# Kernel tuning notes

Hardware: AMD Instinct MI355X
Metric: run time of the kernel (lower is better)

The kernel has to match this reference:

```python
import jax, jax.numpy as jnp
import numpy as np

N, E, IN_DIM, OUT_DIM, R = 100000, 1600000, 128, 128, 8


def setup_inputs() -> dict:
    key = jax.random.key(0)
    k = jax.random.split(key, 6)
    scale_rel = np.sqrt(6.0 / (IN_DIM + OUT_DIM))  # xavier_uniform bound
    x = jax.random.normal(k[0], (N, IN_DIM), dtype=jnp.float32)
    edge_index = jax.random.randint(k[1], (2, E), 0, N, dtype=jnp.int64)
    edge_type = jax.random.randint(k[2], (E,), 0, R, dtype=jnp.int64)
    rel_weight = jax.random.uniform(k[3], (R, IN_DIM, OUT_DIM), dtype=jnp.float32,
                                    minval=-scale_rel, maxval=scale_rel)
    w_self = jax.random.uniform(k[4], (IN_DIM, OUT_DIM), dtype=jnp.float32,
                                minval=-scale_rel, maxval=scale_rel)
    b_self = jax.random.normal(k[5], (OUT_DIM,), dtype=jnp.float32) * 0.01
    return {"x": x, "edge_index": edge_index, "edge_type": edge_type,
            "rel_weight": rel_weight, "w_self": w_self, "b_self": b_self}


def reference(x, edge_index, edge_type, rel_weight, w_self, b_self):
    n = x.shape[0]
    src, dst = edge_index[0], edge_index[1]
    # self-loop term: W_self @ h_v + b
    out = x @ w_self + b_self                                  # (N, out)
    # pre-transform every node by every relation, then gather per edge.
    # equivalent to per-relation masked (x[src_r] @ W_r) + scatter_add.
    xw = jnp.einsum('ni,rio->nro', x, rel_weight)               # (N, R, out)
    msg = xw[src, edge_type]                                    # (E, out)
    agg = jax.ops.segment_sum(msg, dst, num_segments=n)         # (N, out)
    deg = jax.ops.segment_sum(jnp.ones(dst.shape[0], x.dtype), dst, num_segments=n)
    deg = jnp.clip(deg, 1.0)[:, None]                           # (N, 1)
    return jax.nn.relu(out + agg / deg)
```

## Files before the change

### kernel.cpp

```cpp
#include <hip/hip_runtime.h>
#include <hip/hip_bf16.h>

typedef __attribute__((ext_vector_type(4))) float f32x4_t;
typedef __attribute__((ext_vector_type(8))) short bf16x8_t;

#define NCLS 8

__device__ __forceinline__ float bf2f(ushort u) {
  return __uint_as_float(((unsigned)u) << 16);
}
__device__ __forceinline__ ushort f2bf(float f) {
  unsigned u = __float_as_uint(f);
  u += 0x7fffu + ((u >> 16) & 1u);
  return (ushort)(u >> 16);
}
__device__ __forceinline__ uint packbf2(float x, float y) {
  return (uint)f2bf(x) | ((uint)f2bf(y) << 16);
}

__global__ void deg2_kernel(const int* __restrict__ dst, int* __restrict__ deg2,
                            int N, long E) {
  long i = (long)blockIdx.x * blockDim.x + threadIdx.x;
  long st = (long)gridDim.x * blockDim.x;
  for (; i < E; i += st) {
    int cls = (int)((i >> 8) & (NCLS - 1));
    atomicAdd(&deg2[(size_t)cls * N + dst[i]], 1);
  }
}

__global__ void nodedeg_kernel(const int* __restrict__ deg2, int* __restrict__ nodedeg, int N) {
  int d = blockIdx.x * 256 + threadIdx.x;
  if (d >= N) return;
  int s = 0;
#pragma unroll
  for (int c = 0; c < NCLS; c++) s += deg2[(size_t)c * N + d];
  nodedeg[d] = s;
}

__global__ __launch_bounds__(256) void scan1(const int* __restrict__ deg, int* __restrict__ starts,
                                             int* __restrict__ bsum, int M) {
  __shared__ int lds[256];
  const int tid = threadIdx.x;
  const int base = blockIdx.x * 1024 + tid * 4;
  int v0 = 0, v1 = 0, v2 = 0, v3 = 0;
  if (base + 3 < M) {
    int4 q = *(const int4*)(deg + base);
    v0 = q.x; v1 = q.y; v2 = q.z; v3 = q.w;
  } else {
    if (base + 0 < M) v0 = deg[base];
    if (base + 1 < M) v1 = deg[base + 1];
    if (base + 2 < M) v2 = deg[base + 2];
    if (base + 3 < M) v3 = deg[base + 3];
  }
  int s = v0 + v1 + v2 + v3;
  lds[tid] = s;
  __syncthreads();
  for (int off = 1; off < 256; off <<= 1) {
    int t = (tid >= off) ? lds[tid - off] : 0;
    __syncthreads();
    lds[tid] += t;
    __syncthreads();
  }
  int p = lds[tid] - s;
  if (tid == 255) bsum[blockIdx.x] = lds[255];
  if (base + 0 < M) starts[base + 0] = p; p += v0;
  if (base + 1 < M) starts[base + 1] = p; p += v1;
  if (base + 2 < M) starts[base + 2] = p; p += v2;
  if (base + 3 < M) starts[base + 3] = p;
}

__global__ __launch_bounds__(256) void scan2(int* __restrict__ bsum, int nb) {
  __shared__ int lds[256];
  const int tid = threadIdx.x;
  const int base = tid * 4;
  int v[4];
#pragma unroll
  for (int j = 0; j < 4; j++) v[j] = (base + j < nb) ? bsum[base + j] : 0;
  int s = v[0] + v[1] + v[2] + v[3];
  lds[tid] = s;
  __syncthreads();
  for (int off = 1; off < 256; off <<= 1) {
    int t = (tid >= off) ? lds[tid - off] : 0;
    __syncthreads();
    lds[tid] += t;
    __syncthreads();
  }
  int p = lds[tid] - s;
#pragma unroll
  for (int j = 0; j < 4; j++) {
    if (base + j < nb) bsum[base + j] = p;
    p += v[j];
  }
}

__global__ void scan3(int* __restrict__ starts, const int* __restrict__ bsum, int M) {
  int i = blockIdx.x * 256 + threadIdx.x;
  if (i < M) starts[i] += bsum[i >> 10];
}

__global__ void cursor_init(const int* __restrict__ deg2, const int* __restrict__ node_starts,
                            int* __restrict__ cursor, int N) {
  int d = blockIdx.x * 256 + threadIdx.x;
  if (d >= N) return;
  int run = node_starts[d];
#pragma unroll
  for (int c = 0; c < NCLS; c++) {
    cursor[(size_t)c * N + d] = run;
    run += deg2[(size_t)c * N + d];
  }
}

__global__ void fill_csr(const int* __restrict__ src, const int* __restrict__ dst,
                         const int* __restrict__ et, int* __restrict__ cursor,
                         uint* __restrict__ packed, int N, long E) {
  long i = (long)blockIdx.x * blockDim.x + threadIdx.x;
  long st = (long)gridDim.x * blockDim.x;
  for (; i < E; i += st) {
    int cls = (int)((i >> 8) & (NCLS - 1));
    int pos = atomicAdd(&cursor[(size_t)cls * N + dst[i]], 1);
    packed[pos] = ((uint)src[i] << 4) | (uint)et[i];
  }
}

__global__ void build_wT(const float* __restrict__ rel, const float* __restrict__ wself,
                         ushort* __restrict__ wT, int R) {
  int id = blockIdx.x * blockDim.x + threadIdx.x;
  int total = (R + 1) * 128 * 128;
  if (id >= total) return;
  int r = id >> 14;
  int rem = id & 16383;
  int o = rem >> 7;
  int i = rem & 127;
  float v = (r < R) ? rel[((size_t)r << 14) + (i << 7) + o] : wself[(i << 7) + o];
  wT[id] = f2bf(v);
}

__global__ void conv_x_kernel(const float* __restrict__ x, ushort* __restrict__ xb, long n4) {
  long i = (long)blockIdx.x * blockDim.x + threadIdx.x;
  long st = (long)gridDim.x * blockDim.x;
  for (; i < n4; i += st) {
    float4 v = ((const float4*)x)[i];
    ushort4 o;
    o.x = f2bf(v.x); o.y = f2bf(v.y); o.z = f2bf(v.z); o.w = f2bf(v.w);
    ((ushort4*)xb)[i] = o;
  }
}

__global__ __launch_bounds__(256) void gather_sum(const uint* __restrict__ packed,
                                                  const int* __restrict__ node_starts,
                                                  const int* __restrict__ nodedeg,
                                                  const ushort* __restrict__ xb,
                                                  ushort* __restrict__ S,
                                                  int N) {
  const int lane = threadIdx.x & 63;
  const int d = blockIdx.x * 4 + (threadIdx.x >> 6);
  if (d >= N) return;

  const int s0 = node_starts[d];
  const int dg = nodedeg[d];
  const int e1 = s0 + dg;

  float a0x = 0, a0y = 0, a1x = 0, a1y = 0, a2x = 0, a2y = 0, a3x = 0, a3y = 0;
  float a4x = 0, a4y = 0, a5x = 0, a5y = 0, a6x = 0, a6y = 0, a7x = 0, a7y = 0;

#define ACCUM(t, vx, vy)                                  \
  switch (t) {                                            \
    case 0: a0x += vx; a0y += vy; break;                  \
    case 1: a1x += vx; a1y += vy; break;                  \
    case 2: a2x += vx; a2y += vy; break;                  \
    case 3: a3x += vx; a3y += vy; break;                  \
    case 4: a4x += vx; a4y += vy; break;                  \
    case 5: a5x += vx; a5y += vy; break;                  \
    case 6: a6x += vx; a6y += vy; break;                  \
    default: a7x += vx; a7y += vy; break;                 \
  }

  int e = s0;
  for (; e + 3 < e1; e += 4) {
    uint r0 = packed[e], r1 = packed[e + 1], r2 = packed[e + 2], r3 = packed[e + 3];
    ushort2 m0 = *(const ushort2*)(xb + (size_t)(r0 >> 4) * 128 + lane * 2);
    ushort2 m1 = *(const ushort2*)(xb + (size_t)(r1 >> 4) * 128 + lane * 2);
    ushort2 m2 = *(const ushort2*)(xb + (size_t)(r2 >> 4) * 128 + lane * 2);
    ushort2 m3 = *(const ushort2*)(xb + (size_t)(r3 >> 4) * 128 + lane * 2);
    int t0 = (int)(r0 & 15u), t1 = (int)(r1 & 15u);
    int t2 = (int)(r2 & 15u), t3 = (int)(r3 & 15u);
    ACCUM(t0, bf2f(m0.x), bf2f(m0.y));
    ACCUM(t1, bf2f(m1.x), bf2f(m1.y));
    ACCUM(t2, bf2f(m2.x), bf2f(m2.y));
    ACCUM(t3, bf2f(m3.x), bf2f(m3.y));
  }
  for (; e < e1; e++) {
    uint r0 = packed[e];
    ushort2 m0 = *(const ushort2*)(xb + (size_t)(r0 >> 4) * 128 + lane * 2);
    int t0 = (int)(r0 & 15u);
    ACCUM(t0, bf2f(m0.x), bf2f(m0.y));
  }
#undef ACCUM

  const float inv = 1.0f / (float)((dg > 1) ? dg : 1);
  uint* Sd = (uint*)(S + (size_t)d * 1024) + lane;
  __builtin_nontemporal_store(packbf2(a0x * inv, a0y * inv), Sd + 0 * 64);
  __builtin_nontemporal_store(packbf2(a1x * inv, a1y * inv), Sd + 1 * 64);
  __builtin_nontemporal_store(packbf2(a2x * inv, a2y * inv), Sd + 2 * 64);
  __builtin_nontemporal_store(packbf2(a3x * inv, a3y * inv), Sd + 3 * 64);
  __builtin_nontemporal_store(packbf2(a4x * inv, a4y * inv), Sd + 4 * 64);
  __builtin_nontemporal_store(packbf2(a5x * inv, a5y * inv), Sd + 5 * 64);
  __builtin_nontemporal_store(packbf2(a6x * inv, a6y * inv), Sd + 6 * 64);
  __builtin_nontemporal_store(packbf2(a7x * inv, a7y * inv), Sd + 7 * 64);
}

__global__ __launch_bounds__(512) void agg_gemm(const ushort* __restrict__ S,
                                                const ushort* __restrict__ xb,
                                                const ushort* __restrict__ wT,
                                                const float* __restrict__ b,
                                                float* __restrict__ out,
                                                int N, int NR) {
  __shared__ ushort smem[2][16384];

  const int tid = threadIdx.x;
  const int lane = tid & 63;
  const int wave = tid >> 6;
  const int l15 = lane & 15;
  const int l4 = lane >> 4;
  const int nodebase = blockIdx.x * 256 + wave * 32;

  int nd[2], rd[2];
  nd[0] = nodebase + l15;
  nd[1] = nodebase + 16 + l15;
  rd[0] = (nd[0] < N) ? nd[0] : (N - 1);
  rd[1] = (nd[1] < N) ? nd[1] : (N - 1);

  f32x4_t acc[2][8];
#pragma unroll
  for (int g = 0; g < 2; g++)
#pragma unroll
    for (int nt = 0; nt < 8; nt++) acc[g][nt] = {0.f, 0.f, 0.f, 0.f};

  {
    bf16x8_t sreg[4];
#pragma unroll
    for (int j = 0; j < 4; j++) {
      int c = tid + j * 512;
      sreg[j] = *(const bf16x8_t*)(wT + c * 8);
    }
#pragma unroll
    for (int j = 0; j < 4; j++) {
      int c = tid + j * 512;
      int o = c >> 4;
      int colb = (c & 15) * 16;
      int byte = o * 256 + (colb ^ ((o & 7) << 4));
      *(bf16x8_t*)((char*)smem[0] + byte) = sreg[j];
    }
  }
  __syncthreads();

  for (int r = 0; r < NR; r++) {
    bf16x8_t sf[2][4];
#pragma unroll
    for (int g = 0; g < 2; g++) {
      const ushort* srow = (r < NR - 1) ? (S + ((size_t)rd[g] * 8 + r) * 128 + l4 * 8)
                                        : (xb + (size_t)rd[g] * 128 + l4 * 8);
#pragma unroll
      for (int kk = 0; kk < 4; kk++)
        sf[g][kk] = *(const bf16x8_t*)(srow + kk * 32);
    }

    bf16x8_t sreg[4];
    const bool pf = (r + 1 < NR);
    if (pf) {
      const ushort* wsrc = wT + ((size_t)(r + 1) << 14);
#pragma unroll
      for (int j = 0; j < 4; j++) {
        int c = tid + j * 512;
        sreg[j] = *(const bf16x8_t*)(wsrc + c * 8);
      }
    }

    const char* wbuf = (const char*)smem[r & 1];
#pragma unroll
    for (int nt = 0; nt < 8; nt++) {
      bf16x8_t wf[4];
      const int row = nt * 16 + l15;
      const int swz = (row & 7) << 4;
#pragma unroll
      for (int kk = 0; kk < 4; kk++) {
        int colb = l4 * 16 + kk * 64;
        wf[kk] = *(const bf16x8_t*)(wbuf + row * 256 + (colb ^ swz));
      }
#pragma unroll
      for (int g = 0; g < 2; g++)
#pragma unroll
        for (int kk = 0; kk < 4; kk++)
          acc[g][nt] = __builtin_amdgcn_mfma_f32_16x16x32_bf16(wf[kk], sf[g][kk], acc[g][nt], 0, 0, 0);
    }

    if (pf) {
#pragma unroll
      for (int j = 0; j < 4; j++) {
        int c = tid + j * 512;
        int o = c >> 4;
        int colb = (c & 15) * 16;
        int byte = o * 256 + (colb ^ ((o & 7) << 4));
        *(bf16x8_t*)((char*)smem[(r + 1) & 1] + byte) = sreg[j];
      }
    }
    __syncthreads();
  }

#pragma unroll
  for (int g = 0; g < 2; g++) {
    if (nd[g] < N) {
#pragma unroll
      for (int nt = 0; nt < 8; nt++) {
        float4 bv = *(const float4*)(b + nt * 16 + l4 * 4);
        f32x4_t v = acc[g][nt];
        float4 o;
        o.x = fmaxf(v[0] + bv.x, 0.f);
        o.y = fmaxf(v[1] + bv.y, 0.f);
        o.z = fmaxf(v[2] + bv.z, 0.f);
        o.w = fmaxf(v[3] + bv.w, 0.f);
        *(float4*)(out + (size_t)nd[g] * 128 + nt * 16 + l4 * 4) = o;
      }
    }
  }
}

__global__ void deg_kernel(const int* __restrict__ dst, int* __restrict__ deg, long E) {
  long i = (long)blockIdx.x * blockDim.x + threadIdx.x;
  long st = (long)gridDim.x * blockDim.x;
  for (; i < E; i += st) atomicAdd(&deg[dst[i]], 1);
}
__global__ void naive_edge(const float* __restrict__ x, const int* __restrict__ src,
                           const int* __restrict__ dst, const int* __restrict__ et,
                           const float* __restrict__ rel, float* __restrict__ agg, long E) {
  const int lane = threadIdx.x & 63;
  long wid = ((long)blockIdx.x * blockDim.x + threadIdx.x) >> 6;
  long nw = ((long)gridDim.x * blockDim.x) >> 6;
  for (long e = wid; e < E; e += nw) {
    int s = src[e];
    int d = dst[e];
    int t = et[e];
    const float* xs = x + (size_t)s * 128;
    const float* w = rel + (size_t)t * 128 * 128;
    float a0 = 0.f, a1 = 0.f;
    for (int i = 0; i < 128; i++) {
      float xv = xs[i];
      a0 += xv * w[i * 128 + lane];
      a1 += xv * w[i * 128 + lane + 64];
    }
    atomicAdd(agg + (size_t)d * 128 + lane, a0);
    atomicAdd(agg + (size_t)d * 128 + lane + 64, a1);
  }
}
__global__ void naive_self(const float* __restrict__ x, const float* __restrict__ ws,
                           const float* __restrict__ b, const int* __restrict__ deg,
                           float* __restrict__ out, int N) {
  int v = blockIdx.x;
  int o = threadIdx.x;
  if (v >= N) return;
  const float* xv = x + (size_t)v * 128;
  float acc = b[o];
  for (int i = 0; i < 128; i++) acc += xv[i] * ws[i * 128 + o];
  float dg = (float)max(deg[v], 1);
  float val = acc + out[(size_t)v * 128 + o] / dg;
  out[(size_t)v * 128 + o] = fmaxf(val, 0.f);
}

extern "C" void kernel_launch(void* const* d_in, const int* in_sizes, int n_in,
                              void* d_out, int out_size, void* d_ws, size_t ws_size,
                              hipStream_t stream) {
  const float* x = (const float*)d_in[0];
  const int* ei = (const int*)d_in[1];
  const int* et = (const int*)d_in[2];
  const float* rel = (const float*)d_in[3];
  const float* wself = (const float*)d_in[4];
  const float* bself = (const float*)d_in[5];
  float* out = (float*)d_out;

  const int N = in_sizes[0] / 128;
  const long E = in_sizes[2];
  const int R = in_sizes[3] / (128 * 128);
  const int NR = R + 1;
  const int* srcp = ei;
  const int* dstp = ei + E;

  size_t off = 0;
  auto alloc = [&](size_t bytes) {
    size_t o = off;
    off += (bytes + 255) & ~(size_t)255;
    return o;
  };
  size_t deg2_off = alloc((size_t)NCLS * N * 4);
  size_t nodedeg_off = alloc((size_t)N * 4);
  size_t nstart_off = alloc((size_t)N * 4);
  size_t cursor_off = alloc((size_t)NCLS * N * 4);
  size_t bsum_off = alloc(4096);
  size_t wT_off = alloc((size_t)NR * 128 * 128 * 2);
  size_t packed_off = alloc((size_t)E * 4);
  size_t xb_off = alloc((size_t)N * 128 * 2);
  size_t S_off = alloc((size_t)N * 8 * 128 * 2);
  const bool main_path = (ws_size >= off) && (N <= 1024 * 1024) && (R == 8);

  if (main_path) {
    int* deg2 = (int*)((char*)d_ws + deg2_off);
    int* nodedeg = (int*)((char*)d_ws + nodedeg_off);
    int* nstart = (int*)((char*)d_ws + nstart_off);
    int* cursor = (int*)((char*)d_ws + cursor_off);
    int* bsum = (int*)((char*)d_ws + bsum_off);
    ushort* wT = (ushort*)((char*)d_ws + wT_off);
    uint* packed = (uint*)((char*)d_ws + packed_off);
    ushort* xb = (ushort*)((char*)d_ws + xb_off);
    ushort* S = (ushort*)((char*)d_ws + S_off);

    hipMemsetAsync(deg2, 0, (size_t)NCLS * N * 4, stream);
    deg2_kernel<<<2048, 256, 0, stream>>>(dstp, deg2, N, E);
    nodedeg_kernel<<<(N + 255) / 256, 256, 0, stream>>>(deg2, nodedeg, N);

    const int nb = (N + 1023) / 1024;
    scan1<<<nb, 256, 0, stream>>>(nodedeg, nstart, bsum, N);
    scan2<<<1, 256, 0, stream>>>(bsum, nb);
    scan3<<<(N + 255) / 256, 256, 0, stream>>>(nstart, bsum, N);
    cursor_init<<<(N + 255) / 256, 256, 0, stream>>>(deg2, nstart, cursor, N);
    fill_csr<<<2048, 256, 0, stream>>>(srcp, dstp, et, cursor, packed, N, E);
    conv_x_kernel<<<2048, 256, 0, stream>>>(x, xb, (long)N * 32);
    build_wT<<<(NR * 16384 + 255) / 256, 256, 0, stream>>>(rel, wself, wT, R);
    gather_sum<<<(N + 3) / 4, 256, 0, stream>>>(packed, nstart, nodedeg, xb, S, N);
    agg_gemm<<<(N + 255) / 256, 512, 0, stream>>>(S, xb, wT, bself, out, N, NR);
  } else {
    int* deg = (int*)((char*)d_ws + deg2_off);
    hipMemsetAsync(deg, 0, (size_t)N * 4, stream);
    deg_kernel<<<2048, 256, 0, stream>>>(dstp, deg, E);
    hipMemsetAsync(out, 0, (size_t)out_size * 4, stream);
    naive_edge<<<4096, 256, 0, stream>>>(x, srcp, dstp, et, rel, out, E);
    naive_self<<<N, 128, 0, stream>>>(x, wself, bself, deg, out, N);
  }
}
```

Measured before the change: 463.7 us.

## Bucket CSR fill by class-major segments then reorder into node-major CSR

Measured after the change: 455.0 us. Within noise of the previous version (-1.9%).

```diff
diff --git a/kernel.cpp b/kernel.cpp
--- a/kernel.cpp
+++ b/kernel.cpp
@@ -93,21 +93,19 @@
   }
 }
 
-__global__ void scan3(int* __restrict__ starts, const int* __restrict__ bsum, int M) {
+__global__ void scan3m(int* __restrict__ starts, int* __restrict__ cursor,
+                       const int* __restrict__ bsum, int M) {
+  int i = blockIdx.x * 256 + threadIdx.x;
+  if (i < M) {
+    int v = starts[i] + bsum[i >> 10];
+    starts[i] = v;
+    cursor[i] = v;
+  }
+}
+
+__global__ void scan3n(int* __restrict__ starts, const int* __restrict__ bsum, int M) {
   int i = blockIdx.x * 256 + threadIdx.x;
   if (i < M) starts[i] += bsum[i >> 10];
-}
-
-__global__ void cursor_init(const int* __restrict__ deg2, const int* __restrict__ node_starts,
-                            int* __restrict__ cursor, int N) {
-  int d = blockIdx.x * 256 + threadIdx.x;
-  if (d >= N) return;
-  int run = node_starts[d];
-#pragma unroll
-  for (int c = 0; c < NCLS; c++) {
-    cursor[(size_t)c * N + d] = run;
-    run += deg2[(size_t)c * N + d];
-  }
 }
 
 __global__ void fill_csr(const int* __restrict__ src, const int* __restrict__ dst,
@@ -119,6 +117,21 @@
     int cls = (int)((i >> 8) & (NCLS - 1));
     int pos = atomicAdd(&cursor[(size_t)cls * N + dst[i]], 1);
     packed[pos] = ((uint)src[i] << 4) | (uint)et[i];
+  }
+}
+
+__global__ void reorder_kernel(const uint* __restrict__ pin, uint* __restrict__ pout,
+                               const int* __restrict__ starts2, const int* __restrict__ deg2,
+                               const int* __restrict__ node_starts, int N) {
+  int d = blockIdx.x * 256 + threadIdx.x;
+  if (d >= N) return;
+  int run = node_starts[d];
+#pragma unroll
+  for (int c = 0; c < NCLS; c++) {
+    int s = starts2[(size_t)c * N + d];
+    int len = deg2[(size_t)c * N + d];
+    for (int k = 0; k < len; k++) pout[run + k] = pin[s + k];
+    run += len;
   }
 }
 
@@ -383,6 +396,7 @@
   const int NR = R + 1;
   const int* srcp = ei;
   const int* dstp = ei + E;
+  const int M = NCLS * N;
 
   size_t off = 0;
   auto alloc = [&](size_t bytes) {
@@ -390,38 +404,49 @@
     off += (bytes + 255) & ~(size_t)255;
     return o;
   };
-  size_t deg2_off = alloc((size_t)NCLS * N * 4);
+  size_t deg2_off = alloc((size_t)M * 4);
   size_t nodedeg_off = alloc((size_t)N * 4);
   size_t nstart_off = alloc((size_t)N * 4);
-  size_t cursor_off = alloc((size_t)NCLS * N * 4);
+  size_t starts2_off = alloc((size_t)M * 4);
+  size_t cursor2_off = alloc((size_t)M * 4);
   size_t bsum_off = alloc(4096);
   size_t wT_off = alloc((size_t)NR * 128 * 128 * 2);
+  size_t pcls_off = alloc((size_t)E * 4);
   size_t packed_off = alloc((size_t)E * 4);
   size_t xb_off = alloc((size_t)N * 128 * 2);
   size_t S_off = alloc((size_t)N * 8 * 128 * 2);
-  const bool main_path = (ws_size >= off) && (N <= 1024 * 1024) && (R == 8);
+  const bool main_path = (ws_size >= off) && (M <= 1024 * 1024) && (R == 8);
 
   if (main_path) {
     int* deg2 = (int*)((char*)d_ws + deg2_off);
     int* nodedeg = (int*)((char*)d_ws + nodedeg_off);
     int* nstart = (int*)((char*)d_ws + nstart_off);
-    int* cursor = (int*)((char*)d_ws + cursor_off);
+    int* starts2 = (int*)((char*)d_ws + starts2_off);
+    int* cursor2 = (int*)((char*)d_ws + cursor2_off);
     int* bsum = (int*)((char*)d_ws + bsum_off);
     ushort* wT = (ushort*)((char*)d_ws + wT_off);
+    uint* pcls = (uint*)((char*)d_ws + pcls_off);
     uint* packed = (uint*)((char*)d_ws + packed_off);
     ushort* xb = (ushort*)((char*)d_ws + xb_off);
     ushort* S = (ushort*)((char*)d_ws + S_off);
 
-    hipMemsetAsync(deg2, 0, (size_t)NCLS * N * 4, stream);
+    hipMemsetAsync(deg2, 0, (size_t)M * 4, stream);
     deg2_kernel<<<2048, 256, 0, stream>>>(dstp, deg2, N, E);
     nodedeg_kernel<<<(N + 255) / 256, 256, 0, stream>>>(deg2, nodedeg, N);
 
-    const int nb = (N + 1023) / 1024;
-    scan1<<<nb, 256, 0, stream>>>(nodedeg, nstart, bsum, N);
-    scan2<<<1, 256, 0, stream>>>(bsum, nb);
-    scan3<<<(N + 255) / 256, 256, 0, stream>>>(nstart, bsum, N);
-    cursor_init<<<(N + 255) / 256, 256, 0, stream>>>(deg2, nstart, cursor, N);
-    fill_csr<<<2048, 256, 0, stream>>>(srcp, dstp, et, cursor, packed, N, E);
+    const int nbM = (M + 1023) / 1024;
+    scan1<<<nbM, 256, 0, stream>>>(deg2, starts2, bsum, M);
+    scan2<<<1, 256, 0, stream>>>(bsum, nbM);
+    scan3m<<<(M + 255) / 256, 256, 0, stream>>>(starts2, cursor2, bsum, M);
+
+    const int nbN = (N + 1023) / 1024;
+    scan1<<<nbN, 256, 0, stream>>>(nodedeg, nstart, bsum, N);
+    scan2<<<1, 256, 0, stream>>>(bsum, nbN);
+    scan3n<<<(N + 255) / 256, 256, 0, stream>>>(nstart, bsum, N);
+
+    fill_csr<<<2048, 256, 0, stream>>>(srcp, dstp, et, cursor2, pcls, N, E);
+    reorder_kernel<<<(N + 255) / 256, 256, 0, stream>>>(pcls, packed, starts2, deg2, nstart, N);
+
     conv_x_kernel<<<2048, 256, 0, stream>>>(x, xb, (long)N * 32);
     build_wT<<<(NR * 16384 + 255) / 256, 256, 0, stream>>>(rel, wself, wT, R);
     gather_sum<<<(N + 3) / 4, 256, 0, stream>>>(packed, nstart, nodedeg, xb, S, N);
```
